# Kernel tuning notes

Measured on AMD Instinct MI355X. Metric: run time of the kernel, lower is better.

The kernel has to match this reference:

```python
import jax, jax.numpy as jnp
import numpy as np

DIM = 768
HEADS = 12
HEAD_DIM = DIM // HEADS
B, N = 4, 2048


def setup_inputs() -> dict:
    key = jax.random.key(0)
    ks = jax.random.split(key, 5)
    s = 0.02
    return {
        "x": jax.random.normal(ks[0], (B, N, DIM), dtype=jnp.float32),
        "w_qkv": jax.random.normal(ks[1], (DIM, 3 * DIM), dtype=jnp.float32) * s,
        "b_qkv": jnp.zeros((3 * DIM,), dtype=jnp.float32),
        "w_proj": jax.random.normal(ks[2], (DIM, DIM), dtype=jnp.float32) * s,
        "b_proj": jnp.zeros((DIM,), dtype=jnp.float32),
    }


def reference(x, w_qkv, b_qkv, w_proj, b_proj):
    b, n, c = x.shape
    scale = HEAD_DIM ** -0.5
    qkv = x @ w_qkv + b_qkv                       # [B,N,3C]
    qkv = qkv.reshape(b, n, 3, HEADS, HEAD_DIM)
    q = qkv[:, :, 0].transpose(0, 2, 1, 3)        # [B,H,N,D]
    k = qkv[:, :, 1].transpose(0, 2, 1, 3)
    v = qkv[:, :, 2].transpose(0, 2, 1, 3)
    attn = jnp.einsum("bhqd,bhkd->bhqk", q, k) * scale
    attn = jax.nn.softmax(attn, axis=-1)
    out = jnp.einsum("bhqk,bhkd->bhqd", attn, v)  # [B,H,N,D]
    out = out.transpose(0, 2, 1, 3).reshape(b, n, c)
    return out @ w_proj + b_proj
```

## Files before the change

### kernel.cpp

```cpp
#include <hip/hip_runtime.h>

typedef short sh8 __attribute__((ext_vector_type(8)));
typedef short sh4 __attribute__((ext_vector_type(4)));
typedef float f32x4 __attribute__((ext_vector_type(4)));
typedef float f32x16 __attribute__((ext_vector_type(16)));
typedef unsigned u32x4 __attribute__((ext_vector_type(4)));

extern "C" __device__ float __ocml_native_exp2_f32(float);

__device__ __forceinline__ short f2bf(float f) {
  unsigned u = __builtin_bit_cast(unsigned, f);
  u += 0x7fffu + ((u >> 16) & 1u);
  return (short)(u >> 16);
}

__device__ __forceinline__ void gload16(const short* g, short* l) {
  __builtin_amdgcn_global_load_lds(
      (const __attribute__((address_space(1))) unsigned*)g,
      (__attribute__((address_space(3))) unsigned*)l, 16, 0, 0);
}

__device__ __forceinline__ void wait2_barrier() {
  asm volatile("s_waitcnt vmcnt(2)" ::: "memory");
  __builtin_amdgcn_s_barrier();
  asm volatile("" ::: "memory");
}
__device__ __forceinline__ void wait1_barrier() {
  asm volatile("s_waitcnt vmcnt(1)" ::: "memory");
  __builtin_amdgcn_s_barrier();
  asm volatile("" ::: "memory");
}
__device__ __forceinline__ void wait0_barrier() {
  asm volatile("s_waitcnt vmcnt(0)" ::: "memory");
  __builtin_amdgcn_s_barrier();
  asm volatile("" ::: "memory");
}

__device__ __forceinline__ int xcd_swizzle(int bidl, int nwg) {
  int q = nwg >> 3, rr = nwg & 7;
  int xcd = bidl & 7, idx = bidl >> 3;
  return (xcd < rr ? xcd * (q + 1) : rr * (q + 1) + (xcd - rr) * q) + idx;
}

__global__ void cast_f32_bf16(const float* __restrict__ in, short* __restrict__ out, int n) {
  int i = (blockIdx.x * blockDim.x + threadIdx.x) * 4;
  if (i >= n) return;
  float4 f = *(const float4*)(in + i);
  sh4 o;
  o.x = f2bf(f.x); o.y = f2bf(f.y); o.z = f2bf(f.z); o.w = f2bf(f.w);
  *(sh4*)(out + i) = o;
}

__global__ __launch_bounds__(256) void transpose_cast_t(
    const float* __restrict__ in, short* __restrict__ out, int K, int Nn) {
  __shared__ short Tl[64][72];
  const int t = threadIdx.x;
  const int n0 = blockIdx.x * 64, k0 = blockIdx.y * 64;
  const int kr0 = t >> 4;
  const int nc = (t & 15) * 4;
#pragma unroll
  for (int p = 0; p < 4; p++) {
    int kr = kr0 + p * 16;
    float4 f = *(const float4*)(in + (size_t)(k0 + kr) * Nn + n0 + nc);
    Tl[nc + 0][kr] = f2bf(f.x);
    Tl[nc + 1][kr] = f2bf(f.y);
    Tl[nc + 2][kr] = f2bf(f.z);
    Tl[nc + 3][kr] = f2bf(f.w);
  }
  __syncthreads();
  const int nr0 = t >> 3;
  const int kk = (t & 7) * 8;
#pragma unroll
  for (int p = 0; p < 2; p++) {
    int nr = nr0 + p * 32;
    *(sh8*)(out + (size_t)(n0 + nr) * K + k0 + kk) = *(const sh8*)&Tl[nr][kk];
  }
}

template <int OUTF32>
__global__ __launch_bounds__(256, 4) void gemm_bt(
    const short* __restrict__ A, const short* __restrict__ Bt,
    const float* __restrict__ bias, void* __restrict__ Cv,
    int M, int Nn, int K) {
  __shared__ short SMEM[14336];
  const int t = threadIdx.x;
  const int wave = t >> 6, lane = t & 63, quad = lane >> 4, l15 = lane & 15;
  const int wm = (wave >> 1) * 32, wn = (wave & 1) * 64;
  const int nwg = gridDim.x * gridDim.y;
  const int wg = xcd_swizzle(blockIdx.y * gridDim.x + blockIdx.x, nwg);
  const int row0 = (wg / gridDim.x) * 64, col0 = (wg % gridDim.x) * 128;
  f32x4 acc[2][4] = {};

  const int srow = t >> 2;
  const int ssl = ((t & 3) ^ ((t >> 3) & 3)) * 8;
  const short* Asrc0 = A + (size_t)(row0 + srow) * K + ssl;
  const short* Bsrc0 = Bt + (size_t)(col0 + srow) * K + ssl;
  const short* Bsrc1 = Bt + (size_t)(col0 + 64 + srow) * K + ssl;
  short* AsF = SMEM;
  short* BsF = SMEM + 6144;
  const int wdst = wave * 512;

  const int soA = (quad ^ ((l15 >> 1) & 3)) * 8;

  const int T = K >> 5;
  gload16(Asrc0, AsF + wdst);
  gload16(Bsrc0, BsF + wdst);
  gload16(Bsrc1, BsF + 2048 + wdst);
  gload16(Asrc0 + 32, AsF + 2048 + wdst);

  int ra = 0, wa = 2;
  for (int tt = 0; tt < T; tt++) {
    if (tt + 1 < T) wait1_barrier(); else wait0_barrier();
    if (tt + 1 < T) {
      const int k0 = (tt + 1) * 32;
      short* Bd = BsF + ((tt + 1) & 1) * 4096 + wdst;
      gload16(Bsrc0 + k0, Bd);
      gload16(Bsrc1 + k0, Bd + 2048);
    }
    if (tt + 2 < T) {
      gload16(Asrc0 + (tt + 2) * 32, AsF + wa * 2048 + wdst);
    }
    const short* Ab = AsF + ra * 2048;
    const short* Bb = BsF + (tt & 1) * 4096;
    sh8 af[2], bfv[4];
#pragma unroll
    for (int i = 0; i < 2; i++) af[i] = *(const sh8*)&Ab[(wm + i * 16 + l15) * 32 + soA];
#pragma unroll
    for (int j = 0; j < 4; j++) bfv[j] = *(const sh8*)&Bb[(wn + j * 16 + l15) * 32 + soA];
#pragma unroll
    for (int i = 0; i < 2; i++)
#pragma unroll
      for (int j = 0; j < 4; j++)
        acc[i][j] = __builtin_amdgcn_mfma_f32_16x16x32_bf16(af[i], bfv[j], acc[i][j], 0, 0, 0);
    ra = ra == 2 ? 0 : ra + 1;
    wa = wa == 2 ? 0 : wa + 1;
  }

#pragma unroll
  for (int i = 0; i < 2; i++)
#pragma unroll
    for (int j = 0; j < 4; j++) {
      int r = row0 + wm + i * 16 + quad * 4;
      int c = col0 + wn + j * 16 + l15;
      float bv = bias[c];
#pragma unroll
      for (int e = 0; e < 4; e++) {
        float v = acc[i][j][e] + bv;
        if (OUTF32)
          ((float*)Cv)[(size_t)(r + e) * Nn + c] = v;
        else
          ((short*)Cv)[(size_t)(r + e) * Nn + c] = f2bf(v);
      }
    }
}

__global__ __launch_bounds__(256, 4) void gemm_qkv(
    const short* __restrict__ A, const short* __restrict__ Bt,
    const float* __restrict__ bias,
    short* __restrict__ Qh, short* __restrict__ Kh, short* __restrict__ VhT) {
  const int K = 768;
  __shared__ short SMEM[20480];
  const int t = threadIdx.x;
  const int wave = t >> 6, lane = t & 63, quad = lane >> 4, l15 = lane & 15;
  const int wm = (wave >> 1) * 64, wn = (wave & 1) * 64;
  const int nwg = gridDim.x * gridDim.y;
  const int wg = xcd_swizzle(blockIdx.y * gridDim.x + blockIdx.x, nwg);
  const int row0 = (wg / gridDim.x) * 128, col0 = (wg % gridDim.x) * 128;
  f32x4 acc[4][4] = {};

  const int srow = t >> 2;
  const int ssl = ((t & 3) ^ ((t >> 3) & 3)) * 8;
  const short* Asrc0 = A + (size_t)(row0 + srow) * K + ssl;
  const short* Asrc1 = A + (size_t)(row0 + 64 + srow) * K + ssl;
  const short* Bsrc0 = Bt + (size_t)(col0 + srow) * K + ssl;
  const short* Bsrc1 = Bt + (size_t)(col0 + 64 + srow) * K + ssl;
  short* AsF = SMEM;
  short* BsF = SMEM + 12288;
  const int wdst = wave * 512;

  const int soA = (quad ^ ((l15 >> 1) & 3)) * 8;

  const int T = K >> 5;
  gload16(Asrc0, AsF + wdst);
  gload16(Asrc1, AsF + 2048 + wdst);
  gload16(Bsrc0, BsF + wdst);
  gload16(Bsrc1, BsF + 2048 + wdst);
  gload16(Asrc0 + 32, AsF + 4096 + wdst);
  gload16(Asrc1 + 32, AsF + 4096 + 2048 + wdst);

  int ra = 0, wa = 2;
  for (int tt = 0; tt < T; tt++) {
    if (tt + 1 < T) wait2_barrier(); else wait0_barrier();
    if (tt + 1 < T) {
      const int k0 = (tt + 1) * 32;
      short* Bd = BsF + ((tt + 1) & 1) * 4096 + wdst;
      gload16(Bsrc0 + k0, Bd);
      gload16(Bsrc1 + k0, Bd + 2048);
    }
    if (tt + 2 < T) {
      const int k0 = (tt + 2) * 32;
      short* Ad = AsF + wa * 4096 + wdst;
      gload16(Asrc0 + k0, Ad);
      gload16(Asrc1 + k0, Ad + 2048);
    }
    const short* Ab = AsF + ra * 4096;
    const short* Bb = BsF + (tt & 1) * 4096;
    sh8 af[4], bfv[4];
#pragma unroll
    for (int i = 0; i < 4; i++) af[i] = *(const sh8*)&Ab[(wm + i * 16 + l15) * 32 + soA];
#pragma unroll
    for (int j = 0; j < 4; j++) bfv[j] = *(const sh8*)&Bb[(wn + j * 16 + l15) * 32 + soA];
#pragma unroll
    for (int i = 0; i < 4; i++)
#pragma unroll
      for (int j = 0; j < 4; j++)
        acc[i][j] = __builtin_amdgcn_mfma_f32_16x16x32_bf16(af[i], bfv[j], acc[i][j], 0, 0, 0);
    ra = ra == 2 ? 0 : ra + 1;
    wa = wa == 2 ? 0 : wa + 1;
  }

  const int s = col0 >= 1536 ? 2 : (col0 >= 768 ? 1 : 0);

  if (s < 2) {
    short* dst = s == 0 ? Qh : Kh;
    const float scl = (s == 0) ? 0.18033688011112042f : 1.0f;
#pragma unroll
    for (int j = 0; j < 4; j++) {
      int c = col0 + wn + j * 16 + l15;
      int hd = c - s * 768;
      int h = hd >> 6;
      float bv = bias[c];
#pragma unroll
      for (int i = 0; i < 4; i++) {
        int rbase = row0 + wm + i * 16 + quad * 4;
#pragma unroll
        for (int e = 0; e < 4; e++) {
          int r = rbase + e;
          int b = r >> 11, n = r & 2047;
          float v = (acc[i][j][e] + bv) * scl;
          dst[(size_t)(b * 12 + h) * 131072 + n * 64 + (hd & 63)] = f2bf(v);
        }
      }
    }
  } else {
    __syncthreads();
    short* Tl = SMEM;
#pragma unroll
    for (int j = 0; j < 4; j++) {
      int cl = wn + j * 16 + l15;
      float bv = bias[col0 + cl];
#pragma unroll
      for (int i = 0; i < 4; i++) {
        int rl = wm + i * 16 + quad * 4;
        sh4 pk;
#pragma unroll
        for (int e = 0; e < 4; e++) pk[e] = f2bf(acc[i][j][e] + bv);
        *(sh4*)&Tl[cl * 136 + rl] = pk;
      }
    }
    __syncthreads();
    const int b = row0 >> 11, n0 = row0 & 2047;
    const int h0 = (col0 - 1536) >> 6;
#pragma unroll
    for (int p = 0; p < 8; p++) {
      int cl = (t >> 4) + p * 16;
      int nn = (t & 15) * 8;
      int hg = h0 + (cl >> 6);
      int d = cl & 63;
      sh8 vv = *(const sh8*)&Tl[cl * 136 + nn];
      *(sh8*)&VhT[(size_t)(b * 12 + hg) * 131072 + (size_t)d * 2048 + n0 + nn] = vv;
    }
  }
}

__global__ __launch_bounds__(512, 4) void attn9(const short* __restrict__ Qh,
                                                const short* __restrict__ Kh,
                                                const short* __restrict__ VhT,
                                                short* __restrict__ outb) {
  const int bid = blockIdx.x;
  const int qb = bid / 48;
  const int bh = bid - qb * 48;
  const int t = threadIdx.x;
  const int w = t >> 6, lane = t & 63;
  const int wl = w & 3, g = w >> 2;
  const int l31 = lane & 31, hi = lane >> 5;

  __shared__ short SM[40960];

  const size_t hb = (size_t)bh * 131072;

  sh8 qa[4];
  {
    const short* qp = Qh + hb + (size_t)(qb * 128 + wl * 32 + l31) * 64 + hi * 8;
    qa[0] = *(const sh8*)(qp);
    qa[1] = *(const sh8*)(qp + 16);
    qa[2] = *(const sh8*)(qp + 32);
    qa[3] = *(const sh8*)(qp + 48);
  }
  asm volatile("s_waitcnt vmcnt(0)" ::: "memory");

  f32x16 o[2] = {};
  f32x4 lsv = {};

  const int tg = t & 255;
  const int srow = tg >> 3;
  const int ssl = ((tg & 7) ^ (srow & 7)) * 8;
  const short* Ksrc = Kh + hb + (size_t)(g * 1024 + srow) * 64 + ssl;
  const short* Vsrc = VhT + hb + (size_t)srow * 2048 + g * 1024 + ssl;
  short* KlF = SM + g * 20480;
  short* VtF = KlF + 12288;
  const int wdst = wl * 512;

  const int sw7 = l31 & 7;
  int rsl[4];
#pragma unroll
  for (int ks = 0; ks < 4; ks++) rsl[ks] = (((ks << 1) | hi) ^ sw7) * 8;

  gload16(Ksrc, KlF + wdst);
  gload16(Ksrc + (size_t)32 * 64, KlF + 2048 + wdst);
  gload16(Vsrc, VtF + wdst);
  gload16(Vsrc + (size_t)32 * 2048, VtF + 2048 + wdst);
  gload16(Ksrc + (size_t)64 * 64, KlF + 4096 + wdst);
  gload16(Ksrc + (size_t)96 * 64, KlF + 4096 + 2048 + wdst);

  int rk = 0, wk = 2;
  for (int kt = 0; kt < 16; kt++) {
    if (kt < 15) wait2_barrier(); else wait0_barrier();
    if (kt + 1 < 16) {
      const int key0 = (kt + 1) * 64;
      short* Vd = VtF + ((kt + 1) & 1) * 4096 + wdst;
      gload16(Vsrc + key0, Vd);
      gload16(Vsrc + (size_t)32 * 2048 + key0, Vd + 2048);
    }
    if (kt + 2 < 16) {
      const int key0 = (kt + 2) * 64;
      short* Kd = KlF + wk * 4096 + wdst;
      gload16(Ksrc + (size_t)key0 * 64, Kd);
      gload16(Ksrc + (size_t)(key0 + 32) * 64, Kd + 2048);
    }

    const short* Kb = KlF + rk * 4096;
    const short* Vb = VtF + (kt & 1) * 4096;

    sh8 pa[4];
#pragma unroll
    for (int kb = 0; kb < 2; kb++) {
      const short* kr = Kb + (kb * 32 + l31) * 64;
      f32x16 s = {};
#pragma unroll
      for (int ks = 0; ks < 4; ks++)
        s = __builtin_amdgcn_mfma_f32_32x32x16_bf16(*(const sh8*)(kr + rsl[ks]), qa[ks], s, 0, 0, 0);
      unsigned u[8];
#pragma unroll
      for (int m = 0; m < 8; m++) {
        float e0 = __ocml_native_exp2_f32(s[2 * m]);
        float e1 = __ocml_native_exp2_f32(s[2 * m + 1]);
        lsv[m & 3] += e0 + e1;
        asm("v_cvt_pk_bf16_f32 %0, %1, %2" : "=v"(u[m]) : "v"(e0), "v"(e1));
      }
      unsigned y0 = (unsigned)__shfl_xor((int)(hi ? u[0] : u[2]), 32, 64);
      unsigned y1 = (unsigned)__shfl_xor((int)(hi ? u[1] : u[3]), 32, 64);
      unsigned y2 = (unsigned)__shfl_xor((int)(hi ? u[4] : u[6]), 32, 64);
      unsigned y3 = (unsigned)__shfl_xor((int)(hi ? u[5] : u[7]), 32, 64);
      unsigned w0 = hi ? y0 : u[0];
      unsigned w1 = hi ? y1 : u[1];
      unsigned w2 = hi ? u[2] : y0;
      unsigned w3 = hi ? u[3] : y1;
      unsigned w4 = hi ? y2 : u[4];
      unsigned w5 = hi ? y3 : u[5];
      unsigned w6 = hi ? u[6] : y2;
      unsigned w7 = hi ? u[7] : y3;
      u32x4 A0 = {w0, w1, w2, w3};
      u32x4 A1 = {w4, w5, w6, w7};
      pa[2 * kb] = __builtin_bit_cast(sh8, A0);
      pa[2 * kb + 1] = __builtin_bit_cast(sh8, A1);
    }

    __builtin_amdgcn_s_setprio(1);
#pragma unroll
    for (int db = 0; db < 2; db++) {
      const short* vr = Vb + (db * 32 + l31) * 64;
#pragma unroll
      for (int ks = 0; ks < 4; ks++)
        o[db] = __builtin_amdgcn_mfma_f32_32x32x16_bf16(pa[ks], *(const sh8*)(vr + rsl[ks]), o[db], 0, 0, 0);
    }
    __builtin_amdgcn_s_setprio(0);
    rk = rk == 2 ? 0 : rk + 1;
    wk = wk == 2 ? 0 : wk + 1;
  }

  float ls = lsv[0] + lsv[1] + lsv[2] + lsv[3];
  ls += __shfl_xor(ls, 32, 64);

  __syncthreads();
  float* cb = (float*)SM;
  const int ci = (wl * 64 + lane) * 33;
  if (g == 1) {
#pragma unroll
    for (int r = 0; r < 16; r++) {
      cb[ci + r] = o[0][r];
      cb[ci + 16 + r] = o[1][r];
    }
    cb[ci + 32] = ls;
  }
  __syncthreads();
  if (g == 0) {
#pragma unroll
    for (int r = 0; r < 16; r++) {
      o[0][r] += cb[ci + r];
      o[1][r] += cb[ci + 16 + r];
    }
    ls += cb[ci + 32];
    float inv = 1.f / ls;

    const int b = bh / 12, hh = bh - b * 12;
#pragma unroll
    for (int r = 0; r < 16; r++) {
      int qr = (r & 3) + 8 * (r >> 2) + 4 * hi;
      float iv = __shfl(inv, qr, 64);
      int n = qb * 128 + wl * 32 + qr;
      short* op = outb + (size_t)(b * 2048 + n) * 768 + hh * 64 + l31;
      op[0] = f2bf(o[0][r] * iv);
      op[32] = f2bf(o[1][r] * iv);
    }
  }
}

extern "C" void kernel_launch(void* const* d_in, const int* in_sizes, int n_in,
                              void* d_out, int out_size, void* d_ws, size_t ws_size,
                              hipStream_t stream) {
  const float* x = (const float*)d_in[0];
  const float* w_qkv = (const float*)d_in[1];
  const float* b_qkv = (const float*)d_in[2];
  const float* w_proj = (const float*)d_in[3];
  const float* b_proj = (const float*)d_in[4];
  float* out = (float*)d_out;

  char* p = (char*)d_ws;
  short* xb = (short*)p;     p += (size_t)8192 * 768 * 2;
  short* wqkvT = (short*)p;  p += (size_t)2304 * 768 * 2;
  short* wprojT = (short*)p; p += (size_t)768 * 768 * 2;
  short* Qh = (short*)p;     p += (size_t)48 * 131072 * 2;
  short* Kh = (short*)p;     p += (size_t)48 * 131072 * 2;
  short* VhT = (short*)p;    p += (size_t)48 * 131072 * 2;
  short* attnb = (short*)p;  p += (size_t)8192 * 768 * 2;

  cast_f32_bf16<<<(8192 * 768 / 4) / 256, 256, 0, stream>>>(x, xb, 8192 * 768);
  {
    dim3 gt(2304 / 64, 768 / 64);
    transpose_cast_t<<<gt, 256, 0, stream>>>(w_qkv, wqkvT, 768, 2304);
  }
  {
    dim3 gt(768 / 64, 768 / 64);
    transpose_cast_t<<<gt, 256, 0, stream>>>(w_proj, wprojT, 768, 768);
  }

  dim3 g1(2304 / 128, 8192 / 128);
  gemm_qkv<<<g1, 256, 0, stream>>>(xb, wqkvT, b_qkv, Qh, Kh, VhT);

  attn9<<<16 * 48, 512, 0, stream>>>(Qh, Kh, VhT, attnb);

  dim3 g2(768 / 128, 8192 / 64);
  gemm_bt<1><<<g2, 256, 0, stream>>>(attnb, wprojT, b_proj, out, 8192, 768, 768);
}
```

Before: 222.6 us.

## Software-pipeline attention PV with next QK; enlarge projection GEMM tile

The attention loop now defers each tile's P·V MFMAs to the next iteration, so they run while the following tile's QK^T and exp work is in flight. K moves to double buffering and V to triple buffering, with a tail step for the last tile. Separately, the output-projection GEMM goes from 64x128 to 128x128 tiles, giving each wave 4x4 accumulators. This raises data reuse but halves the block count (384 blocks) and adds register and LDS pressure.

```diff
diff --git a/kernel.cpp b/kernel.cpp
--- a/kernel.cpp
+++ b/kernel.cpp
@@ -22,11 +22,6 @@
 
 __device__ __forceinline__ void wait2_barrier() {
   asm volatile("s_waitcnt vmcnt(2)" ::: "memory");
-  __builtin_amdgcn_s_barrier();
-  asm volatile("" ::: "memory");
-}
-__device__ __forceinline__ void wait1_barrier() {
-  asm volatile("s_waitcnt vmcnt(1)" ::: "memory");
   __builtin_amdgcn_s_barrier();
   asm volatile("" ::: "memory");
 }
@@ -82,35 +77,38 @@
     const short* __restrict__ A, const short* __restrict__ Bt,
     const float* __restrict__ bias, void* __restrict__ Cv,
     int M, int Nn, int K) {
-  __shared__ short SMEM[14336];
+  __shared__ short SMEM[20480];
   const int t = threadIdx.x;
   const int wave = t >> 6, lane = t & 63, quad = lane >> 4, l15 = lane & 15;
-  const int wm = (wave >> 1) * 32, wn = (wave & 1) * 64;
+  const int wm = (wave >> 1) * 64, wn = (wave & 1) * 64;
   const int nwg = gridDim.x * gridDim.y;
   const int wg = xcd_swizzle(blockIdx.y * gridDim.x + blockIdx.x, nwg);
-  const int row0 = (wg / gridDim.x) * 64, col0 = (wg % gridDim.x) * 128;
-  f32x4 acc[2][4] = {};
+  const int row0 = (wg / gridDim.x) * 128, col0 = (wg % gridDim.x) * 128;
+  f32x4 acc[4][4] = {};
 
   const int srow = t >> 2;
   const int ssl = ((t & 3) ^ ((t >> 3) & 3)) * 8;
   const short* Asrc0 = A + (size_t)(row0 + srow) * K + ssl;
+  const short* Asrc1 = A + (size_t)(row0 + 64 + srow) * K + ssl;
   const short* Bsrc0 = Bt + (size_t)(col0 + srow) * K + ssl;
   const short* Bsrc1 = Bt + (size_t)(col0 + 64 + srow) * K + ssl;
   short* AsF = SMEM;
-  short* BsF = SMEM + 6144;
+  short* BsF = SMEM + 12288;
   const int wdst = wave * 512;
 
   const int soA = (quad ^ ((l15 >> 1) & 3)) * 8;
 
   const int T = K >> 5;
   gload16(Asrc0, AsF + wdst);
+  gload16(Asrc1, AsF + 2048 + wdst);
   gload16(Bsrc0, BsF + wdst);
   gload16(Bsrc1, BsF + 2048 + wdst);
-  gload16(Asrc0 + 32, AsF + 2048 + wdst);
+  gload16(Asrc0 + 32, AsF + 4096 + wdst);
+  gload16(Asrc1 + 32, AsF + 4096 + 2048 + wdst);
 
   int ra = 0, wa = 2;
   for (int tt = 0; tt < T; tt++) {
-    if (tt + 1 < T) wait1_barrier(); else wait0_barrier();
+    if (tt + 1 < T) wait2_barrier(); else wait0_barrier();
     if (tt + 1 < T) {
       const int k0 = (tt + 1) * 32;
       short* Bd = BsF + ((tt + 1) & 1) * 4096 + wdst;
@@ -118,17 +116,20 @@
       gload16(Bsrc1 + k0, Bd + 2048);
     }
     if (tt + 2 < T) {
-      gload16(Asrc0 + (tt + 2) * 32, AsF + wa * 2048 + wdst);
-    }
-    const short* Ab = AsF + ra * 2048;
+      const int k0 = (tt + 2) * 32;
+      short* Ad = AsF + wa * 4096 + wdst;
+      gload16(Asrc0 + k0, Ad);
+      gload16(Asrc1 + k0, Ad + 2048);
+    }
+    const short* Ab = AsF + ra * 4096;
     const short* Bb = BsF + (tt & 1) * 4096;
-    sh8 af[2], bfv[4];
-#pragma unroll
-    for (int i = 0; i < 2; i++) af[i] = *(const sh8*)&Ab[(wm + i * 16 + l15) * 32 + soA];
+    sh8 af[4], bfv[4];
+#pragma unroll
+    for (int i = 0; i < 4; i++) af[i] = *(const sh8*)&Ab[(wm + i * 16 + l15) * 32 + soA];
 #pragma unroll
     for (int j = 0; j < 4; j++) bfv[j] = *(const sh8*)&Bb[(wn + j * 16 + l15) * 32 + soA];
 #pragma unroll
-    for (int i = 0; i < 2; i++)
+    for (int i = 0; i < 4; i++)
 #pragma unroll
       for (int j = 0; j < 4; j++)
         acc[i][j] = __builtin_amdgcn_mfma_f32_16x16x32_bf16(af[i], bfv[j], acc[i][j], 0, 0, 0);
@@ -137,7 +138,7 @@
   }
 
 #pragma unroll
-  for (int i = 0; i < 2; i++)
+  for (int i = 0; i < 4; i++)
 #pragma unroll
     for (int j = 0; j < 4; j++) {
       int r = row0 + wm + i * 16 + quad * 4;
@@ -273,10 +274,10 @@
   }
 }
 
-__global__ __launch_bounds__(512, 4) void attn9(const short* __restrict__ Qh,
-                                                const short* __restrict__ Kh,
-                                                const short* __restrict__ VhT,
-                                                short* __restrict__ outb) {
+__global__ __launch_bounds__(512, 4) void attn10(const short* __restrict__ Qh,
+                                                 const short* __restrict__ Kh,
+                                                 const short* __restrict__ VhT,
+                                                 short* __restrict__ outb) {
   const int bid = blockIdx.x;
   const int qb = bid / 48;
   const int bh = bid - qb * 48;
@@ -308,7 +309,7 @@
   const short* Ksrc = Kh + hb + (size_t)(g * 1024 + srow) * 64 + ssl;
   const short* Vsrc = VhT + hb + (size_t)srow * 2048 + g * 1024 + ssl;
   short* KlF = SM + g * 20480;
-  short* VtF = KlF + 12288;
+  short* VtF = KlF + 8192;
   const int wdst = wl * 512;
 
   const int sw7 = l31 & 7;
@@ -320,29 +321,26 @@
   gload16(Ksrc + (size_t)32 * 64, KlF + 2048 + wdst);
   gload16(Vsrc, VtF + wdst);
   gload16(Vsrc + (size_t)32 * 2048, VtF + 2048 + wdst);
-  gload16(Ksrc + (size_t)64 * 64, KlF + 4096 + wdst);
-  gload16(Ksrc + (size_t)96 * 64, KlF + 4096 + 2048 + wdst);
-
-  int rk = 0, wk = 2;
+
+  sh8 pap[4] = {};
+  int vw = 1;
+  int vp = 2;
+
   for (int kt = 0; kt < 16; kt++) {
-    if (kt < 15) wait2_barrier(); else wait0_barrier();
+    wait2_barrier();
     if (kt + 1 < 16) {
       const int key0 = (kt + 1) * 64;
-      short* Vd = VtF + ((kt + 1) & 1) * 4096 + wdst;
+      short* Kd = KlF + ((kt + 1) & 1) * 4096 + wdst;
+      gload16(Ksrc + (size_t)key0 * 64, Kd);
+      gload16(Ksrc + (size_t)(key0 + 32) * 64, Kd + 2048);
+      short* Vd = VtF + vw * 4096 + wdst;
       gload16(Vsrc + key0, Vd);
       gload16(Vsrc + (size_t)32 * 2048 + key0, Vd + 2048);
     }
-    if (kt + 2 < 16) {
-      const int key0 = (kt + 2) * 64;
-      short* Kd = KlF + wk * 4096 + wdst;
-      gload16(Ksrc + (size_t)key0 * 64, Kd);
-      gload16(Ksrc + (size_t)(key0 + 32) * 64, Kd + 2048);
-    }
-
-    const short* Kb = KlF + rk * 4096;
-    const short* Vb = VtF + (kt & 1) * 4096;
-
-    sh8 pa[4];
+
+    const short* Kb = KlF + (kt & 1) * 4096;
+
+    unsigned u0[8], u1[8];
 #pragma unroll
     for (int kb = 0; kb < 2; kb++) {
       const short* kr = Kb + (kb * 32 + l31) * 64;
@@ -350,43 +348,64 @@
 #pragma unroll
       for (int ks = 0; ks < 4; ks++)
         s = __builtin_amdgcn_mfma_f32_32x32x16_bf16(*(const sh8*)(kr + rsl[ks]), qa[ks], s, 0, 0, 0);
-      unsigned u[8];
+      unsigned* uu = kb ? u1 : u0;
 #pragma unroll
       for (int m = 0; m < 8; m++) {
         float e0 = __ocml_native_exp2_f32(s[2 * m]);
         float e1 = __ocml_native_exp2_f32(s[2 * m + 1]);
         lsv[m & 3] += e0 + e1;
-        asm("v_cvt_pk_bf16_f32 %0, %1, %2" : "=v"(u[m]) : "v"(e0), "v"(e1));
+        asm("v_cvt_pk_bf16_f32 %0, %1, %2" : "=v"(uu[m]) : "v"(e0), "v"(e1));
       }
-      unsigned y0 = (unsigned)__shfl_xor((int)(hi ? u[0] : u[2]), 32, 64);
-      unsigned y1 = (unsigned)__shfl_xor((int)(hi ? u[1] : u[3]), 32, 64);
-      unsigned y2 = (unsigned)__shfl_xor((int)(hi ? u[4] : u[6]), 32, 64);
-      unsigned y3 = (unsigned)__shfl_xor((int)(hi ? u[5] : u[7]), 32, 64);
-      unsigned w0 = hi ? y0 : u[0];
-      unsigned w1 = hi ? y1 : u[1];
-      unsigned w2 = hi ? u[2] : y0;
-      unsigned w3 = hi ? u[3] : y1;
-      unsigned w4 = hi ? y2 : u[4];
-      unsigned w5 = hi ? y3 : u[5];
-      unsigned w6 = hi ? u[6] : y2;
-      unsigned w7 = hi ? u[7] : y3;
+    }
+
+    if (kt > 0) {
+      const short* Vb = VtF + vp * 4096;
+      __builtin_amdgcn_s_setprio(1);
+#pragma unroll
+      for (int db = 0; db < 2; db++) {
+        const short* vr = Vb + (db * 32 + l31) * 64;
+#pragma unroll
+        for (int ks = 0; ks < 4; ks++)
+          o[db] = __builtin_amdgcn_mfma_f32_32x32x16_bf16(pap[ks], *(const sh8*)(vr + rsl[ks]), o[db], 0, 0, 0);
+      }
+      __builtin_amdgcn_s_setprio(0);
+    }
+
+#pragma unroll
+    for (int kb = 0; kb < 2; kb++) {
+      const unsigned* uu = kb ? u1 : u0;
+      unsigned y0 = (unsigned)__shfl_xor((int)(hi ? uu[0] : uu[2]), 32, 64);
+      unsigned y1 = (unsigned)__shfl_xor((int)(hi ? uu[1] : uu[3]), 32, 64);
+      unsigned y2 = (unsigned)__shfl_xor((int)(hi ? uu[4] : uu[6]), 32, 64);
+      unsigned y3 = (unsigned)__shfl_xor((int)(hi ? uu[5] : uu[7]), 32, 64);
+      unsigned w0 = hi ? y0 : uu[0];
+      unsigned w1 = hi ? y1 : uu[1];
+      unsigned w2 = hi ? uu[2] : y0;
+      unsigned w3 = hi ? uu[3] : y1;
+      unsigned w4 = hi ? y2 : uu[4];
+      unsigned w5 = hi ? y3 : uu[5];
+      unsigned w6 = hi ? uu[6] : y2;
+      unsigned w7 = hi ? uu[7] : y3;
       u32x4 A0 = {w0, w1, w2, w3};
       u32x4 A1 = {w4, w5, w6, w7};
-      pa[2 * kb] = __builtin_bit_cast(sh8, A0);
-      pa[2 * kb + 1] = __builtin_bit_cast(sh8, A1);
-    }
-
-    __builtin_amdgcn_s_setprio(1);
+      pap[2 * kb] = __builtin_bit_cast(sh8, A0);
+      pap[2 * kb + 1] = __builtin_bit_cast(sh8, A1);
+    }
+
+    vw = vw == 2 ? 0 : vw + 1;
+    vp = vp == 2 ? 0 : vp + 1;
+  }
+
+  wait0_barrier();
+  {
+    const short* Vb = VtF;
 #pragma unroll
     for (int db = 0; db < 2; db++) {
       const short* vr = Vb + (db * 32 + l31) * 64;
 #pragma unroll
       for (int ks = 0; ks < 4; ks++)
-        o[db] = __builtin_amdgcn_mfma_f32_32x32x16_bf16(pa[ks], *(const sh8*)(vr + rsl[ks]), o[db], 0, 0, 0);
-    }
-    __builtin_amdgcn_s_setprio(0);
-    rk = rk == 2 ? 0 : rk + 1;
-    wk = wk == 2 ? 0 : wk + 1;
+        o[db] = __builtin_amdgcn_mfma_f32_32x32x16_bf16(pap[ks], *(const sh8*)(vr + rsl[ks]), o[db], 0, 0, 0);
+    }
   }
 
   float ls = lsv[0] + lsv[1] + lsv[2] + lsv[3];
@@ -458,8 +477,8 @@
   dim3 g1(2304 / 128, 8192 / 128);
   gemm_qkv<<<g1, 256, 0, stream>>>(xb, wqkvT, b_qkv, Qh, Kh, VhT);
 
-  attn9<<<16 * 48, 512, 0, stream>>>(Qh, Kh, VhT, attnb);
-
-  dim3 g2(768 / 128, 8192 / 64);
+  attn10<<<16 * 48, 512, 0, stream>>>(Qh, Kh, VhT, attnb);
+
+  dim3 g2(768 / 128, 8192 / 128);
   gemm_bt<1><<<g2, 256, 0, stream>>>(attnb, wprojT, b_proj, out, 8192, 768, 768);
 }
```

After: 214.5 us. -3.6%, faster.
